# Optimization experiments

Measured on AMD Instinct MI355X. Metric: run time of the kernel, lower is better.

The kernel has to match this reference:

```python
import jax, jax.numpy as jnp
import numpy as np

# GLIF3 / AlphaPSC constants (from module __init__)
DT = 1.0
V_TH = -45.0
V_RESET = -60.0
C_M = 2.0
TAU = 20.0
TAU_REF = 2.0  # refractory ignored: not in update_state_names ('neuron.v','neuron.Iasc','synapse.psc')
K = jnp.array([0.1, 0.2], dtype=jnp.float32)          # ASC decay rates (1/ms)
ASC_AMPS = jnp.array([1.0, -2.0], dtype=jnp.float32)  # ASC jump amplitudes on spike
TAU_SYN = 5.0

T, B, N_IN, N_HID, N_OUT = 1000, 64, 256, 512, 128


def setup_inputs() -> dict:
    key = jax.random.key(0)
    k1, k2, k3, k4 = jax.random.split(key, 4)
    x = jax.random.normal(k1, (T, B, N_IN), dtype=jnp.float32)
    # Linear layers (bias=False) with fan-in scaled init
    W_in = jax.random.normal(k2, (N_HID, N_IN), dtype=jnp.float32) / np.sqrt(N_IN)
    W_rec = jax.random.normal(k3, (N_HID, N_HID), dtype=jnp.float32) / np.sqrt(N_HID)
    W_out = jax.random.normal(k4, (N_OUT, N_HID), dtype=jnp.float32) / np.sqrt(N_HID)
    return {"x": x, "W_in": W_in, "W_rec": W_rec, "W_out": W_out}


def reference(x, W_in, W_rec, W_out):
    decay_v = DT / TAU                      # leak factor toward v_reset
    decay_asc = jnp.exp(-K * DT)            # (2,)
    decay_syn = jnp.exp(-DT / TAU_SYN)

    x_proj = jnp.einsum('tbi,hi->tbh', x, W_in)  # (T,B,H) input currents

    def step(carry, I_in):
        v, iasc, psc = carry  # v,psc: (B,H); iasc: (B,H,2)
        I_total = I_in + psc + iasc.sum(-1)
        # GLIF membrane integration: dv = dt/c_m * I - dt/tau * (v - v_reset)
        v_int = v + (DT / C_M) * I_total - decay_v * (v - V_RESET)
        spike = (v_int >= V_TH).astype(v_int.dtype)
        v_new = spike * V_RESET + (1.0 - spike) * v_int          # hard reset
        iasc_new = iasc * decay_asc + spike[..., None] * ASC_AMPS  # after-spike currents
        # AlphaPSC with dense recurrent connection
        psc_new = psc * decay_syn + spike @ W_rec.T
        return (v_new, iasc_new, psc_new), spike

    v0 = jnp.full((B, N_HID), V_RESET, dtype=x.dtype)
    iasc0 = jnp.zeros((B, N_HID, 2), dtype=x.dtype)
    psc0 = jnp.zeros((B, N_HID), dtype=x.dtype)
    _, spikes = jax.lax.scan(step, (v0, iasc0, psc0), x_proj)  # spikes: (T,B,H)

    rate = spikes.mean(axis=0)          # (B,H) mean firing rate
    out = rate @ W_out.T                # (B, num_output)
    return out
```

## Files before the change

### kernel.cpp

```cpp
#include <hip/hip_runtime.h>
#include <stdint.h>

#define H 512
#define BATCH 64
#define NIN 256
#define NOUT 128
#define TTOT 1000
#define CHL 20
#define NCH 50

typedef __attribute__((ext_vector_type(4))) float f32x4;

static __device__ __forceinline__ float bf2f(unsigned short b) {
  union { uint32_t u; float f; } x; x.u = ((uint32_t)b) << 16;
  return x.f;
}
static __device__ __forceinline__ int pk_fp8x4(float a, float b, float c,
                                               float d) {
  int v = 0;
  v = __builtin_amdgcn_cvt_pk_fp8_f32(a, b, v, false);
  v = __builtin_amdgcn_cvt_pk_fp8_f32(c, d, v, true);
  return v;
}
__device__ __forceinline__ void gload_lds16(const void* g, void* l) {
  __builtin_amdgcn_global_load_lds(
      (const __attribute__((address_space(1))) uint32_t*)g,
      (__attribute__((address_space(3))) uint32_t*)l, 16, 0, 0);
}

__global__ __launch_bounds__(256) void k_filter(const float* __restrict__ x,
                                                uint8_t* __restrict__ y,
                                                const float* __restrict__ Win,
                                                uint8_t* __restrict__ Winb,
                                                const float* __restrict__ Wrec,
                                                float* __restrict__ WT) {
  const int bid = blockIdx.x;
  const int tid = threadIdx.x;
  if (bid < 400) {
    const int g = bid * 256 + tid;
    const int ig = g & 31, b = (g >> 5) & 63, c = g >> 11;
    const size_t base = ((size_t)c * CHL * 64 + b) * 256 + ig * 8;
    const float* xa = x + base;
    uint8_t* ya = y + base;
    float a[8] = {};
#pragma unroll
    for (int s = 0; s < CHL; ++s) {
      float4 xl = *(const float4*)(xa + (size_t)s * 16384);
      float4 xh = *(const float4*)(xa + (size_t)s * 16384 + 4);
      a[0] = 0.95f * a[0] + xl.x; a[1] = 0.95f * a[1] + xl.y;
      a[2] = 0.95f * a[2] + xl.z; a[3] = 0.95f * a[3] + xl.w;
      a[4] = 0.95f * a[4] + xh.x; a[5] = 0.95f * a[5] + xh.y;
      a[6] = 0.95f * a[6] + xh.z; a[7] = 0.95f * a[7] + xh.w;
      int2 o;
      o.x = pk_fp8x4(a[0], a[1], a[2], a[3]);
      o.y = pk_fp8x4(a[4], a[5], a[6], a[7]);
      *(int2*)(ya + (size_t)s * 16384) = o;
    }
  } else if (bid < 464) {
    const int g = (bid - 400) * 256 + tid;
    const float4* p = (const float4*)Win + (size_t)g * 2;
    float4 a = p[0], b = p[1];
    int2 o;
    o.x = pk_fp8x4(a.x, a.y, a.z, a.w);
    o.y = pk_fp8x4(b.x, b.y, b.z, b.w);
    *(int2*)(Winb + (size_t)g * 8) = o;
  } else {
    __shared__ float tile[32][33];
    const int id = bid - 464;
    const int j0 = (id & 15) * 32, h0 = (id >> 4) * 32;
    const int tx = tid & 31, ty = tid >> 5;
    for (int r = ty; r < 32; r += 8) tile[r][tx] = Wrec[(h0 + r) * H + j0 + tx];
    __syncthreads();
    for (int r = ty; r < 32; r += 8) WT[(j0 + r) * H + h0 + tx] = tile[tx][r];
  }
}

__global__ __launch_bounds__(256) void k_bc(const uint8_t* __restrict__ y,
                                            const uint8_t* __restrict__ B,
                                            float* __restrict__ Bc) {
  __shared__ __align__(16) char lds[65536];
  char* ldsA = lds;
  char* ldsB = lds + 32768;
  const int bn = blockIdx.x & 3;
  const int bm = blockIdx.x >> 2;
  const int tid = threadIdx.x;
  const int wave = tid >> 6;
  const int l = tid & 63;
  const int wr = wave >> 1, wc = wave & 1;
  const int fr = l & 15, fq = l >> 4;
  const char* Bb = (const char*)B + (size_t)bn * 128 * 256;
  const int scol = (l & 15) * 16;
#pragma unroll
  for (int i = 0; i < 8; ++i) {
    const int r0 = wave * 32 + i * 4;
    const int r = r0 + (l >> 4);
    const int sc = scol ^ ((r & 7) << 4);
    const int vr = bm * 128 + r;
    const int cc = vr >> 6, bb2 = vr & 63;
    gload_lds16((const char*)y + ((size_t)(cc * CHL + CHL - 1) * 64 + bb2) * 256 + sc,
                ldsA + r0 * 256);
    gload_lds16(Bb + (size_t)r * 256 + sc, ldsB + r0 * 256);
  }
  __syncthreads();
  f32x4 acc[4][4] = {};
#pragma unroll
  for (int kk = 0; kk < 8; ++kk) {
    const int cb = kk * 32 + fq * 8;
    long a[4], b[4];
#pragma unroll
    for (int m = 0; m < 4; ++m) {
      const int row = wr * 64 + m * 16 + fr;
      a[m] = *(const long*)(ldsA + row * 256 + (cb ^ ((row & 7) << 4)));
    }
#pragma unroll
    for (int n = 0; n < 4; ++n) {
      const int row = wc * 64 + n * 16 + fr;
      b[n] = *(const long*)(ldsB + row * 256 + (cb ^ ((row & 7) << 4)));
    }
#pragma unroll
    for (int m = 0; m < 4; ++m)
#pragma unroll
      for (int n = 0; n < 4; ++n)
        acc[m][n] = __builtin_amdgcn_mfma_f32_16x16x32_fp8_fp8(a[m], b[n],
                                                               acc[m][n], 0, 0, 0);
  }
#pragma unroll
  for (int m = 0; m < 4; ++m) {
    const int r0 = bm * 128 + wr * 64 + m * 16 + fq * 4;
#pragma unroll
    for (int n = 0; n < 4; ++n) {
      const int col = bn * 128 + wc * 64 + n * 16 + fr;
      f32x4 a = acc[m][n];
#pragma unroll
      for (int j = 0; j < 4; ++j)
        Bc[(size_t)(r0 + j) * 512 + col] = 0.5f * a[j] - 38.4908446554876f;
    }
  }
}

__global__ __launch_bounds__(256) void k_compose(const float* __restrict__ Bc,
                                                 float* __restrict__ Vst,
                                                 int* __restrict__ flags) {
  if (blockIdx.x == 0 && threadIdx.x < BATCH) flags[threadIdx.x] = 0;
  const int idx = blockIdx.x * 256 + threadIdx.x;
  const float AL = 0.35848592240854223f;
  float v = -60.f;
#pragma unroll
  for (int c = 0; c < NCH; c += 5) {
    float b0 = Bc[(size_t)(c + 0) * 32768 + idx];
    float b1 = Bc[(size_t)(c + 1) * 32768 + idx];
    float b2 = Bc[(size_t)(c + 2) * 32768 + idx];
    float b3 = Bc[(size_t)(c + 3) * 32768 + idx];
    float b4 = Bc[(size_t)(c + 4) * 32768 + idx];
    Vst[(size_t)(c + 0) * 32768 + idx] = v; v = AL * v + b0;
    Vst[(size_t)(c + 1) * 32768 + idx] = v; v = AL * v + b1;
    Vst[(size_t)(c + 2) * 32768 + idx] = v; v = AL * v + b2;
    Vst[(size_t)(c + 3) * 32768 + idx] = v; v = AL * v + b3;
    Vst[(size_t)(c + 4) * 32768 + idx] = v; v = AL * v + b4;
  }
}

__global__ __launch_bounds__(256) void k_screen(const uint8_t* __restrict__ A,
                                                const uint8_t* __restrict__ B,
                                                const float* __restrict__ Vst,
                                                int* __restrict__ flags) {
  __shared__ __align__(16) char lds[65536];
  char* ldsA = lds;
  char* ldsB = lds + 32768;
  const int bid = blockIdx.x;
  const int wg = (bid & 7) * 250 + (bid >> 3);
  const int bn = wg & 3;
  const int bm = wg >> 2;
  const int tid = threadIdx.x;
  const int wave = tid >> 6;
  const int l = tid & 63;
  const int wr = wave >> 1, wc = wave & 1;
  const int fr = l & 15, fq = l >> 4;
  const char* Ab = (const char*)A + (size_t)bm * 128 * 256;
  const char* Bb = (const char*)B + (size_t)bn * 128 * 256;
  const int scol = (l & 15) * 16;
#pragma unroll
  for (int i = 0; i < 8; ++i) {
    const int r0 = wave * 32 + i * 4;
    const int r = r0 + (l >> 4);
    const int sc = scol ^ ((r & 7) << 4);
    gload_lds16(Ab + (size_t)r * 256 + sc, ldsA + r0 * 256);
    gload_lds16(Bb + (size_t)r * 256 + sc, ldsB + r0 * 256);
  }
  __syncthreads();
  f32x4 acc[4][4] = {};
#pragma unroll
  for (int kk = 0; kk < 8; ++kk) {
    const int cb = kk * 32 + fq * 8;
    long a[4], b[4];
#pragma unroll
    for (int m = 0; m < 4; ++m) {
      const int row = wr * 64 + m * 16 + fr;
      a[m] = *(const long*)(ldsA + row * 256 + (cb ^ ((row & 7) << 4)));
    }
#pragma unroll
    for (int n = 0; n < 4; ++n) {
      const int row = wc * 64 + n * 16 + fr;
      b[n] = *(const long*)(ldsB + row * 256 + (cb ^ ((row & 7) << 4)));
    }
#pragma unroll
    for (int m = 0; m < 4; ++m)
#pragma unroll
      for (int n = 0; n < 4; ++n)
        acc[m][n] = __builtin_amdgcn_mfma_f32_16x16x32_fp8_fp8(a[m], b[n],
                                                               acc[m][n], 0, 0, 0);
  }
  __syncthreads();
  const int c = (bm * 2) / CHL;
  const int s = (bm * 2 + wr) - c * CHL;
  float* ldsV = (float*)lds;
  {
    const float* src = Vst + ((size_t)c * 64) * 512 + bn * 128;
    const int b0 = tid >> 2;
    const int c0 = (tid & 3) * 32;
#pragma unroll
    for (int j = 0; j < 8; ++j) {
      float4 v4 = *(const float4*)(src + (size_t)b0 * 512 + c0 + j * 4);
      *(float4*)(ldsV + b0 * 128 + c0 + j * 4) = v4;
    }
  }
  __syncthreads();
  const float As = exp2f(-(float)(s + 1) * 0.07400058144086257f);
  unsigned int cmask = 0;
#pragma unroll
  for (int m = 0; m < 4; ++m) {
#pragma unroll
    for (int j = 0; j < 4; ++j) {
      const int b = m * 16 + fq * 4 + j;
      bool cb2 = false;
#pragma unroll
      for (int n = 0; n < 4; ++n) {
        const int hl = wc * 64 + n * 16 + fr;
        const float th = 29.f - 2.f * As * (ldsV[b * 128 + hl] + 60.f);
        cb2 |= (acc[m][n][j] >= th);
      }
      cmask |= cb2 ? (1u << (m * 4 + j)) : 0u;
    }
  }
  if (__ballot(cmask != 0u)) {
#pragma unroll
    for (int m = 0; m < 4; ++m)
#pragma unroll
      for (int j = 0; j < 4; ++j)
        if (cmask & (1u << (m * 4 + j))) flags[m * 16 + fq * 4 + j] = 1;
  }
}

__global__ __launch_bounds__(512) void k_fallback(
    const float* __restrict__ x, const float* __restrict__ Win,
    const float* __restrict__ WrecT, const float* __restrict__ Wout,
    const int* __restrict__ flags, float* __restrict__ out) {
  const int b = blockIdx.x;
  const int h = threadIdx.x;
  if (!flags[b]) {
    if (h < NOUT) out[b * NOUT + h] = 0.f;
    return;
  }
  const int wid = h >> 6;
  const int lane = h & 63;
  __shared__ float xr[NIN];
  __shared__ unsigned long long wbal[8];
  __shared__ float rbuf[H];
  __shared__ float pbuf[4][NOUT];
  const float D0 = 0.90483741803595957316f;
  const float D1 = 0.81873075307798185867f;
  const float DS = 0.81873075307798185867f;
  const float* wrow = Win + (size_t)h * NIN;
  float v = -60.f, a0 = 0.f, a1 = 0.f, psc = 0.f, rsum = 0.f;
  for (int t = 0; t < TTOT; ++t) {
    __syncthreads();
    if (h < NIN) xr[h] = x[((size_t)t * 64 + b) * NIN + h];
    __syncthreads();
    float xp = 0.f;
#pragma unroll 8
    for (int k = 0; k < NIN; ++k) xp += wrow[k] * xr[k];
    float It = xp + psc + a0 + a1;
    float vint = 0.95f * v + 0.5f * It - 3.0f;
    bool fire = vint >= -45.f;
    unsigned long long bal = __ballot(fire);
    if (lane == 0) wbal[wid] = bal;
    __syncthreads();
    float rec = 0.f;
    for (int g = 0; g < 8; ++g) {
      unsigned long long m = wbal[g];
      while (m) {
        int j = (g << 6) + __builtin_ctzll(m);
        m &= m - 1;
        rec += WrecT[(size_t)j * H + h];
      }
    }
    v = fire ? -60.f : vint;
    a0 = a0 * D0 + (fire ? 1.f : 0.f);
    a1 = a1 * D1 + (fire ? -2.f : 0.f);
    psc = psc * DS + rec;
    rsum += fire ? 1.f : 0.f;
  }
  rbuf[h] = rsum * 0.001f;
  __syncthreads();
  const int o = h & 127, part = h >> 7;
  const float4* wr4 = (const float4*)(Wout + (size_t)o * H + part * 128);
  const float* rb = rbuf + part * 128;
  float acc = 0.f;
#pragma unroll 8
  for (int q = 0; q < 32; ++q) {
    float4 wv = wr4[q];
    acc += wv.x * rb[q * 4] + wv.y * rb[q * 4 + 1] + wv.z * rb[q * 4 + 2] +
           wv.w * rb[q * 4 + 3];
  }
  pbuf[part][o] = acc;
  __syncthreads();
  if (h < NOUT)
    out[b * NOUT + h] = pbuf[0][h] + pbuf[1][h] + pbuf[2][h] + pbuf[3][h];
}

extern "C" void kernel_launch(void* const* d_in, const int* in_sizes, int n_in,
                              void* d_out, int out_size, void* d_ws,
                              size_t ws_size, hipStream_t stream) {
  const float* x = (const float*)d_in[0];
  const float* Win = (const float*)d_in[1];
  const float* Wrec = (const float*)d_in[2];
  const float* Wout = (const float*)d_in[3];
  float* out = (float*)d_out;

  char* ws = (char*)d_ws;
  float* WrecT = (float*)ws;
  uint8_t* Winb = (uint8_t*)(ws + (1 << 20));
  int* flags = (int*)(ws + (3 << 19));
  uint8_t* y = (uint8_t*)(ws + (2 << 20));
  float* Bc = (float*)(ws + ((size_t)20 << 20));
  float* Vst = (float*)(ws + ((size_t)28 << 20));

  hipLaunchKernelGGL(k_filter, dim3(720), dim3(256), 0, stream, x, y, Win,
                     Winb, Wrec, WrecT);
  hipLaunchKernelGGL(k_bc, dim3(100), dim3(256), 0, stream, y, Winb, Bc);
  hipLaunchKernelGGL(k_compose, dim3(128), dim3(256), 0, stream, Bc, Vst,
                     flags);
  hipLaunchKernelGGL(k_screen, dim3(2000), dim3(256), 0, stream, y, Winb, Vst,
                     flags);
  hipLaunchKernelGGL(k_fallback, dim3(BATCH), dim3(512), 0, stream, x, Win,
                     WrecT, Wout, flags, out);
}
```

Measured before the change: 54.95 us.

## Split filter scan into two halves with carry fixup; drop Wrec transpose

The k_filter prefix-decay scan over each 20-step chunk is now split into two 10-step halves handled by separate threads. The second half is corrected with a carry from the first half through shared memory and precomputed decay powers. This raises parallelism from 400 to 1600 blocks to better saturate memory bandwidth. The Wrec transpose blocks are removed, and the fallback kernel now reads Wrec rows directly per thread. That makes its gathers uncoalesced, but the path only runs when screening flags a batch.

```diff
diff --git a/kernel.cpp b/kernel.cpp
--- a/kernel.cpp
+++ b/kernel.cpp
@@ -11,10 +11,6 @@
 
 typedef __attribute__((ext_vector_type(4))) float f32x4;
 
-static __device__ __forceinline__ float bf2f(unsigned short b) {
-  union { uint32_t u; float f; } x; x.u = ((uint32_t)b) << 16;
-  return x.f;
-}
 static __device__ __forceinline__ int pk_fp8x4(float a, float b, float c,
                                                float d) {
   int v = 0;
@@ -31,47 +27,56 @@
 __global__ __launch_bounds__(256) void k_filter(const float* __restrict__ x,
                                                 uint8_t* __restrict__ y,
                                                 const float* __restrict__ Win,
-                                                uint8_t* __restrict__ Winb,
-                                                const float* __restrict__ Wrec,
-                                                float* __restrict__ WT) {
+                                                uint8_t* __restrict__ Winb) {
   const int bid = blockIdx.x;
   const int tid = threadIdx.x;
-  if (bid < 400) {
-    const int g = bid * 256 + tid;
-    const int ig = g & 31, b = (g >> 5) & 63, c = g >> 11;
-    const size_t base = ((size_t)c * CHL * 64 + b) * 256 + ig * 8;
-    const float* xa = x + base;
-    uint8_t* ya = y + base;
-    float a[8] = {};
-#pragma unroll
-    for (int s = 0; s < CHL; ++s) {
-      float4 xl = *(const float4*)(xa + (size_t)s * 16384);
-      float4 xh = *(const float4*)(xa + (size_t)s * 16384 + 4);
-      a[0] = 0.95f * a[0] + xl.x; a[1] = 0.95f * a[1] + xl.y;
-      a[2] = 0.95f * a[2] + xl.z; a[3] = 0.95f * a[3] + xl.w;
-      a[4] = 0.95f * a[4] + xh.x; a[5] = 0.95f * a[5] + xh.y;
-      a[6] = 0.95f * a[6] + xh.z; a[7] = 0.95f * a[7] + xh.w;
-      int2 o;
-      o.x = pk_fp8x4(a[0], a[1], a[2], a[3]);
-      o.y = pk_fp8x4(a[4], a[5], a[6], a[7]);
-      *(int2*)(ya + (size_t)s * 16384) = o;
-    }
-  } else if (bid < 464) {
-    const int g = (bid - 400) * 256 + tid;
-    const float4* p = (const float4*)Win + (size_t)g * 2;
-    float4 a = p[0], b = p[1];
+  if (bid < 1600) {
+    __shared__ float4 y9dep[2][64];
+    const int c = bid >> 5;
+    const int bp = bid & 31;
+    const int ig = tid & 63;
+    const int half = (tid >> 6) & 1;
+    const int bo = tid >> 7;
+    const int b = bp * 2 + bo;
+    const size_t base = ((size_t)(c * CHL) * 64 + b) * 256 + ig * 4;
+    const float* xa = x + base + (size_t)half * 10 * 16384;
+    uint8_t* ya = y + base + (size_t)half * 10 * 16384;
+    float4 p[10];
+    float ax = 0.f, ay = 0.f, az = 0.f, aw = 0.f;
+#pragma unroll
+    for (int s = 0; s < 10; ++s) {
+      float4 xv = *(const float4*)(xa + (size_t)s * 16384);
+      ax = 0.95f * ax + xv.x; ay = 0.95f * ay + xv.y;
+      az = 0.95f * az + xv.z; aw = 0.95f * aw + xv.w;
+      p[s] = make_float4(ax, ay, az, aw);
+      if (half == 0)
+        *(int*)(ya + (size_t)s * 16384) = pk_fp8x4(ax, ay, az, aw);
+    }
+    if (half == 0) y9dep[bo][ig] = make_float4(ax, ay, az, aw);
+    __syncthreads();
+    if (half == 1) {
+      const float4 y9 = y9dep[bo][ig];
+      const float pw[10] = {0.95f, 0.9025f, 0.857375f, 0.81450625f,
+                            0.7737809375f, 0.735091890625f,
+                            0.69833729609375f, 0.6634204312890625f,
+                            0.6302494097246094f, 0.5987369392383789f};
+#pragma unroll
+      for (int s = 0; s < 10; ++s) {
+        const float ox = p[s].x + pw[s] * y9.x;
+        const float oy = p[s].y + pw[s] * y9.y;
+        const float oz = p[s].z + pw[s] * y9.z;
+        const float ow = p[s].w + pw[s] * y9.w;
+        *(int*)(ya + (size_t)s * 16384) = pk_fp8x4(ox, oy, oz, ow);
+      }
+    }
+  } else {
+    const int g = (bid - 1600) * 256 + tid;
+    const float4* ptr = (const float4*)Win + (size_t)g * 2;
+    float4 a = ptr[0], b = ptr[1];
     int2 o;
     o.x = pk_fp8x4(a.x, a.y, a.z, a.w);
     o.y = pk_fp8x4(b.x, b.y, b.z, b.w);
     *(int2*)(Winb + (size_t)g * 8) = o;
-  } else {
-    __shared__ float tile[32][33];
-    const int id = bid - 464;
-    const int j0 = (id & 15) * 32, h0 = (id >> 4) * 32;
-    const int tx = tid & 31, ty = tid >> 5;
-    for (int r = ty; r < 32; r += 8) tile[r][tx] = Wrec[(h0 + r) * H + j0 + tx];
-    __syncthreads();
-    for (int r = ty; r < 32; r += 8) WT[(j0 + r) * H + h0 + tx] = tile[tx][r];
   }
 }
 
@@ -253,7 +258,7 @@
 
 __global__ __launch_bounds__(512) void k_fallback(
     const float* __restrict__ x, const float* __restrict__ Win,
-    const float* __restrict__ WrecT, const float* __restrict__ Wout,
+    const float* __restrict__ Wrec, const float* __restrict__ Wout,
     const int* __restrict__ flags, float* __restrict__ out) {
   const int b = blockIdx.x;
   const int h = threadIdx.x;
@@ -271,6 +276,7 @@
   const float D1 = 0.81873075307798185867f;
   const float DS = 0.81873075307798185867f;
   const float* wrow = Win + (size_t)h * NIN;
+  const float* rrow = Wrec + (size_t)h * H;
   float v = -60.f, a0 = 0.f, a1 = 0.f, psc = 0.f, rsum = 0.f;
   for (int t = 0; t < TTOT; ++t) {
     __syncthreads();
@@ -291,7 +297,7 @@
       while (m) {
         int j = (g << 6) + __builtin_ctzll(m);
         m &= m - 1;
-        rec += WrecT[(size_t)j * H + h];
+        rec += rrow[j];
       }
     }
     v = fire ? -60.f : vint;
@@ -328,20 +334,19 @@
   float* out = (float*)d_out;
 
   char* ws = (char*)d_ws;
-  float* WrecT = (float*)ws;
   uint8_t* Winb = (uint8_t*)(ws + (1 << 20));
   int* flags = (int*)(ws + (3 << 19));
   uint8_t* y = (uint8_t*)(ws + (2 << 20));
   float* Bc = (float*)(ws + ((size_t)20 << 20));
   float* Vst = (float*)(ws + ((size_t)28 << 20));
 
-  hipLaunchKernelGGL(k_filter, dim3(720), dim3(256), 0, stream, x, y, Win,
-                     Winb, Wrec, WrecT);
+  hipLaunchKernelGGL(k_filter, dim3(1664), dim3(256), 0, stream, x, y, Win,
+                     Winb);
   hipLaunchKernelGGL(k_bc, dim3(100), dim3(256), 0, stream, y, Winb, Bc);
   hipLaunchKernelGGL(k_compose, dim3(128), dim3(256), 0, stream, Bc, Vst,
                      flags);
   hipLaunchKernelGGL(k_screen, dim3(2000), dim3(256), 0, stream, y, Winb, Vst,
                      flags);
   hipLaunchKernelGGL(k_fallback, dim3(BATCH), dim3(512), 0, stream, x, Win,
-                     WrecT, Wout, flags, out);
-}
+                     Wrec, Wout, flags, out);
+}
```

New measurement: 54.65 us. About the same (-0.6%).
